# Optimization experiments

Measured on AMD Instinct MI355X. Metric: run time of the kernel, lower is better.

The kernel has to match this reference:

```python
import jax, jax.numpy as jnp
import numpy as np

NHEAD = 16
D_MODEL = 1024
HEAD_DIM = D_MODEL // NHEAD


def setup_inputs() -> dict:
    key = jax.random.key(0)
    k1, k2, k3 = jax.random.split(key, 3)
    x = jax.random.normal(k1, (4, 2048, D_MODEL), dtype=jnp.float32)
    # lecun_normal-like scaling for stability
    w_qkv = jax.random.normal(k2, (D_MODEL, 3 * D_MODEL), dtype=jnp.float32) / np.sqrt(D_MODEL)
    w_out = jax.random.normal(k3, (D_MODEL, D_MODEL), dtype=jnp.float32) / np.sqrt(D_MODEL)
    return {"x": x, "w_qkv": w_qkv, "w_out": w_out}


def reference(x, w_qkv, w_out):
    # Fused QKV projection (self-attention: x_kv = x)
    qkv = x @ w_qkv  # [B, S, 3*D]
    q, k, v = jnp.split(qkv, 3, axis=-1)
    B, S = x.shape[0], x.shape[1]
    # [B, S, H, hd] -> [B, H, S, hd]
    q = jnp.moveaxis(q.reshape(B, S, NHEAD, HEAD_DIM), -2, -3)
    k = jnp.moveaxis(k.reshape(B, S, NHEAD, HEAD_DIM), -2, -3)
    v = jnp.moveaxis(v.reshape(B, S, NHEAD, HEAD_DIM), -2, -3)
    scale = 1.0 / jnp.sqrt(jnp.float32(HEAD_DIM))
    logits = jnp.einsum('bhqd,bhkd->bhqk', q, k) * scale
    weights = jax.nn.softmax(logits, axis=-1)
    out = jnp.einsum('bhqk,bhkd->bhqd', weights, v)  # [B, H, S, hd]
    out = jnp.moveaxis(out, -3, -2).reshape(B, S, D_MODEL)
    return out @ w_out
```

## Files before the change

### kernel.cpp

```cpp
#include <hip/hip_runtime.h>
#include <hip/hip_bf16.h>
#include <math.h>

#define D_MODEL 1024
#define NHEAD   16
#define HEAD_DIM 64
#define BATCH   4
#define SEQ     2048

typedef __attribute__((ext_vector_type(8))) short bf16x8;
typedef __attribute__((ext_vector_type(4))) float f32x4;
typedef __attribute__((ext_vector_type(16))) float f32x16;

__device__ inline ushort f2bf(float f) {
  __hip_bfloat16 h = __float2bfloat16(f);
  return *reinterpret_cast<ushort*>(&h);
}
__device__ inline uint pk2(float a, float b) {
  return (uint)f2bf(a) | ((uint)f2bf(b) << 16);
}
__device__ inline float bf2f(ushort u) {
  return __uint_as_float((uint)u << 16);
}
__device__ inline f32x16 zero16() {
  f32x16 z;
#pragma unroll
  for (int i = 0; i < 16; ++i) z[i] = 0.f;
  return z;
}
__device__ inline float fexp2(float x) { return __builtin_amdgcn_exp2f(x); }

__device__ inline void gld_lds16(const ushort* g, ushort* l) {
  __builtin_amdgcn_global_load_lds(
      (const __attribute__((address_space(1))) void*)g,
      (__attribute__((address_space(3))) void*)l, 16, 0, 0);
}

__global__ __launch_bounds__(256) void fill_f32(float* __restrict__ p, int n, float v) {
  int i = blockIdx.x * 256 + threadIdx.x;
  if (i < n) p[i] = v;
}

__global__ __launch_bounds__(256) void cast_bf16(const float* __restrict__ in,
                                                 ushort* __restrict__ out, int n8) {
  int i = blockIdx.x * 256 + threadIdx.x;
  if (i >= n8) return;
  const float4* p = (const float4*)(in + i * 8);
  float4 a = p[0], b = p[1];
  uint4 o;
  o.x = pk2(a.x, a.y); o.y = pk2(a.z, a.w);
  o.z = pk2(b.x, b.y); o.w = pk2(b.z, b.w);
  ((uint4*)out)[i] = o;
}

__global__ __launch_bounds__(256) void transpose_f32_bf16(const float* __restrict__ in,
                                                          ushort* __restrict__ out,
                                                          int R, int C) {
  __shared__ float tile[32][33];
  int tx = threadIdx.x, ty = threadIdx.y;
  int c0 = blockIdx.x * 32, r0 = blockIdx.y * 32;
#pragma unroll
  for (int k = 0; k < 4; ++k)
    tile[ty + 8 * k][tx] = in[(size_t)(r0 + ty + 8 * k) * C + c0 + tx];
  __syncthreads();
#pragma unroll
  for (int k = 0; k < 4; ++k)
    out[(size_t)(c0 + ty + 8 * k) * R + r0 + tx] = f2bf(tile[tx][ty + 8 * k]);
}

template <typename OutT>
__global__ __launch_bounds__(256) void gemm_mfma(const ushort* __restrict__ A,
                                                 const ushort* __restrict__ BT,
                                                 OutT* __restrict__ C,
                                                 int M, int N, int K) {
  __shared__ ushort As[128 * 32];
  __shared__ ushort Bs[128 * 32];

  const int tid = threadIdx.x;
  const int w = tid >> 6, lane = tid & 63;
  const int quad = lane >> 4, l16 = lane & 15;

  int bx = blockIdx.x, by = blockIdx.y;
  {
    int nwg = gridDim.x * gridDim.y;
    if ((nwg & 7) == 0) {
      int bid = by * gridDim.x + bx;
      int chunk = nwg >> 3;
      bid = (bid & 7) * chunk + (bid >> 3);
      bx = bid % gridDim.x;
      by = bid / gridDim.x;
    }
  }
  const int m0 = by * 128, n0 = bx * 128;
  const int wm = (w & 1) * 64, wn = (w >> 1) * 64;

  f32x4 acc[4][4];
#pragma unroll
  for (int mt = 0; mt < 4; ++mt)
#pragma unroll
    for (int nt = 0; nt < 4; ++nt) acc[mt][nt] = (f32x4){0.f, 0.f, 0.f, 0.f};

  const int c0 = w * 64 + lane;
  const int r0a = c0 >> 2, k0a = (c0 & 3) * 8;
  const int c1 = 256 + c0;
  const int r1a = c1 >> 2, k1a = (c1 & 3) * 8;
  const ushort* a_src0 = A + (size_t)(m0 + r0a) * K + k0a;
  const ushort* a_src1 = A + (size_t)(m0 + r1a) * K + k1a;
  const ushort* b_src0 = BT + (size_t)(n0 + r0a) * K + k0a;
  const ushort* b_src1 = BT + (size_t)(n0 + r1a) * K + k1a;
  ushort* a_dst0 = As + (size_t)w * 512;
  ushort* a_dst1 = As + 2048 + (size_t)w * 512;
  ushort* b_dst0 = Bs + (size_t)w * 512;
  ushort* b_dst1 = Bs + 2048 + (size_t)w * 512;

  for (int k0 = 0; k0 < K; k0 += 32) {
    gld_lds16(a_src0 + k0, a_dst0);
    gld_lds16(a_src1 + k0, a_dst1);
    gld_lds16(b_src0 + k0, b_dst0);
    gld_lds16(b_src1 + k0, b_dst1);
    __syncthreads();

    bf16x8 af[4], bf[4];
#pragma unroll
    for (int mt = 0; mt < 4; ++mt)
      af[mt] = *(const bf16x8*)(As + (wm + mt * 16 + l16) * 32 + quad * 8);
#pragma unroll
    for (int nt = 0; nt < 4; ++nt)
      bf[nt] = *(const bf16x8*)(Bs + (wn + nt * 16 + l16) * 32 + quad * 8);
#pragma unroll
    for (int mt = 0; mt < 4; ++mt)
#pragma unroll
      for (int nt = 0; nt < 4; ++nt)
        acc[mt][nt] = __builtin_amdgcn_mfma_f32_16x16x32_bf16(af[mt], bf[nt], acc[mt][nt], 0, 0, 0);
    __syncthreads();
  }

#pragma unroll
  for (int mt = 0; mt < 4; ++mt) {
#pragma unroll
    for (int nt = 0; nt < 4; ++nt) {
#pragma unroll
      for (int r = 0; r < 4; ++r) {
        size_t idx = (size_t)(m0 + wm + mt * 16 + quad * 4 + r) * N + n0 + wn + nt * 16 + l16;
        if constexpr (sizeof(OutT) == 4) C[idx] = acc[mt][nt][r];
        else                             C[idx] = f2bf(acc[mt][nt][r]);
      }
    }
  }
}

#define KST 72
#define VST 72
#define NT  (SEQ / 64)
__global__ __launch_bounds__(256, 4) void attn_mfma(const ushort* __restrict__ qkv,
                                                    ushort* __restrict__ attn_o) {
  __shared__ ushort Ks[2][64 * KST];
  __shared__ ushort VTs[2][64 * VST];

  const int tid = threadIdx.x;
  const int w = tid >> 6, lane = tid & 63;
  const int q32 = lane & 31, hi = lane >> 5;

  const int f = blockIdx.x;
  const int xcd = f & 7;
  const int j = f >> 3;
  const int qb = j & 15;
  const int hb = ((j >> 4) << 3) | xcd;
  const int h = hb & 15, b = hb >> 4;
  const int q0 = qb * 128;

  const float qscale = 0.125f * 1.44269504088896f;
  bf16x8 qfrag[4];
  {
    const ushort* qrow = qkv + (size_t)(b * SEQ + q0 + w * 32 + q32) * 3072 + h * 64;
#pragma unroll
    for (int dd = 0; dd < 4; ++dd) {
      bf16x8 fq = *(const bf16x8*)(qrow + dd * 16 + hi * 8);
#pragma unroll
      for (int jj = 0; jj < 8; ++jj)
        fq[jj] = (short)f2bf(bf2f((ushort)fq[jj]) * qscale);
      qfrag[dd] = fq;
    }
  }

  f32x16 oacc0 = zero16(), oacc1 = zero16(), lacc = zero16();

  bf16x8 ones;
#pragma unroll
  for (int jj = 0; jj < 8; ++jj) ones[jj] = (short)0x3F80;

  const int sr = tid >> 2, sc = tid & 3;
  const int kp = tid & 31, dg = tid >> 5;

  const size_t kstep = (size_t)64 * 3072;
  const ushort* kbase = qkv + (size_t)(b * SEQ + sr) * 3072 + 1024 + h * 64 + sc * 16;
  const ushort* vbase = qkv + (size_t)(b * SEQ + 2 * kp) * 3072 + 2048 + h * 64 + dg * 8;

  uint4 kreg0, kreg1, vreg0, vreg1;
  {
    const uint4* ks = (const uint4*)kbase;
    kreg0 = ks[0]; kreg1 = ks[1];
    vreg0 = *(const uint4*)vbase;
    vreg1 = *(const uint4*)(vbase + 3072);
    uint4* kdst = (uint4*)(Ks[0] + sr * KST + sc * 16);
    kdst[0] = kreg0; kdst[1] = kreg1;
    const ushort* ae = (const ushort*)&vreg0;
    const ushort* ce = (const ushort*)&vreg1;
#pragma unroll
    for (int jj = 0; jj < 8; ++jj) {
      VTs[0][(dg * 8 + jj) * VST + 2 * kp]     = ae[jj];
      VTs[0][(dg * 8 + jj) * VST + 2 * kp + 1] = ce[jj];
    }
  }

  for (int kt = 0; kt < NT; ++kt) {
    const int cur = kt & 1;
    __syncthreads();

    if (kt + 1 < NT) {
      const uint4* ks = (const uint4*)(kbase + (size_t)(kt + 1) * kstep);
      kreg0 = ks[0]; kreg1 = ks[1];
      vreg0 = *(const uint4*)(vbase + (size_t)(kt + 1) * kstep);
      vreg1 = *(const uint4*)(vbase + (size_t)(kt + 1) * kstep + 3072);
    }

    f32x16 sacc0 = zero16(), sacc1 = zero16();
    __builtin_amdgcn_s_setprio(1);
#pragma unroll
    for (int dd = 0; dd < 4; ++dd) {
      bf16x8 kf0 = *(const bf16x8*)(Ks[cur] + (q32)*KST + dd * 16 + hi * 8);
      bf16x8 kf1 = *(const bf16x8*)(Ks[cur] + (32 + q32) * KST + dd * 16 + hi * 8);
      sacc0 = __builtin_amdgcn_mfma_f32_32x32x16_bf16(kf0, qfrag[dd], sacc0, 0, 0, 0);
      sacc1 = __builtin_amdgcn_mfma_f32_32x32x16_bf16(kf1, qfrag[dd], sacc1, 0, 0, 0);
    }
    __builtin_amdgcn_s_setprio(0);

    bf16x8 pa[4];
#pragma unroll
    for (int kblk = 0; kblk < 2; ++kblk) {
      const f32x16& sacc = kblk ? sacc1 : sacc0;
      uint d0[4], d1[4];
#pragma unroll
      for (int p = 0; p < 4; ++p) {
        d0[p] = pk2(fexp2(sacc[4 * p + 0]), fexp2(sacc[4 * p + 1]));
        d1[p] = pk2(fexp2(sacc[4 * p + 2]), fexp2(sacc[4 * p + 3]));
      }
#pragma unroll
      for (int k2 = 0; k2 < 2; ++k2) {
        uint A0 = d0[2 * k2], B0 = d0[2 * k2 + 1];
        uint A1 = d1[2 * k2], B1 = d1[2 * k2 + 1];
        asm("v_permlane32_swap_b32 %0, %1" : "+v"(A0), "+v"(B0));
        asm("v_permlane32_swap_b32 %0, %1" : "+v"(A1), "+v"(B1));
        uint4 fr = {A0, A1, B0, B1};
        pa[kblk * 2 + k2] = *(bf16x8*)&fr;
        lacc = __builtin_amdgcn_mfma_f32_32x32x16_bf16(pa[kblk * 2 + k2], ones, lacc, 0, 0, 0);
      }
    }

    __builtin_amdgcn_s_setprio(1);
#pragma unroll
    for (int kb2 = 0; kb2 < 4; ++kb2) {
      bf16x8 vf0 = *(const bf16x8*)(VTs[cur] + (q32)*VST + kb2 * 16 + hi * 8);
      bf16x8 vf1 = *(const bf16x8*)(VTs[cur] + (32 + q32) * VST + kb2 * 16 + hi * 8);
      oacc0 = __builtin_amdgcn_mfma_f32_32x32x16_bf16(pa[kb2], vf0, oacc0, 0, 0, 0);
      oacc1 = __builtin_amdgcn_mfma_f32_32x32x16_bf16(pa[kb2], vf1, oacc1, 0, 0, 0);
    }
    __builtin_amdgcn_s_setprio(0);

    if (kt + 1 < NT) {
      uint4* kdst = (uint4*)(Ks[cur ^ 1] + sr * KST + sc * 16);
      kdst[0] = kreg0; kdst[1] = kreg1;
      const ushort* ae = (const ushort*)&vreg0;
      const ushort* ce = (const ushort*)&vreg1;
#pragma unroll
      for (int jj = 0; jj < 8; ++jj) {
        VTs[cur ^ 1][(dg * 8 + jj) * VST + 2 * kp]     = ae[jj];
        VTs[cur ^ 1][(dg * 8 + jj) * VST + 2 * kp + 1] = ce[jj];
      }
    }
  }

#pragma unroll
  for (int p = 0; p < 4; ++p) {
#pragma unroll
    for (int r = 0; r < 4; ++r) {
      int qrow = r + 8 * p + 4 * hi;
      float linv = 1.0f / lacc[4 * p + r];
      ushort* orow = attn_o + (size_t)(b * SEQ + q0 + w * 32 + qrow) * 1024 + h * 64 + q32;
      orow[0]  = f2bf(oacc0[4 * p + r] * linv);
      orow[32] = f2bf(oacc1[4 * p + r] * linv);
    }
  }
}

extern "C" void kernel_launch(void* const* d_in, const int* in_sizes, int n_in,
                              void* d_out, int out_size, void* d_ws, size_t ws_size,
                              hipStream_t stream) {
  bool ok_n  = (n_in == 3);
  bool ok_s0 = ok_n && (in_sizes[0] == 4 * 2048 * 1024);
  bool ok_s1 = ok_n && (in_sizes[1] == 1024 * 3072);
  bool ok_s2 = ok_n && (in_sizes[2] == 1024 * 1024);
  bool ok_o  = (out_size == 4 * 2048 * 1024);
  bool ok_w  = (ws_size >= (size_t)8192 * 3072 * 4);
  if (!(ok_n && ok_s0 && ok_s1 && ok_s2 && ok_o && ok_w)) {
    float c = 64.0f + 1.0f * ok_n + 2.0f * ok_s0 + 4.0f * ok_s1 +
              8.0f * ok_s2 + 16.0f * ok_o + 32.0f * ok_w;
    fill_f32<<<(out_size + 255) / 256, 256, 0, stream>>>((float*)d_out, out_size, c);
    return;
  }

  const float* x     = (const float*)d_in[0];
  const float* w_qkv = (const float*)d_in[1];
  const float* w_out = (const float*)d_in[2];

  char* ws = (char*)d_ws;
  ushort* qkv    = (ushort*)ws;
  ushort* xb     = (ushort*)(ws + (size_t)48 * 1024 * 1024);
  ushort* attn_o = (ushort*)(ws + (size_t)64 * 1024 * 1024);
  ushort* wqkvT  = (ushort*)(ws + (size_t)80 * 1024 * 1024);
  ushort* woutT  = (ushort*)(ws + (size_t)86 * 1024 * 1024);

  cast_bf16<<<dim3(8192 * 1024 / 8 / 256), dim3(256), 0, stream>>>(x, xb, 8192 * 1024 / 8);
  transpose_f32_bf16<<<dim3(3072 / 32, 1024 / 32), dim3(32, 8), 0, stream>>>(w_qkv, wqkvT, 1024, 3072);
  transpose_f32_bf16<<<dim3(1024 / 32, 1024 / 32), dim3(32, 8), 0, stream>>>(w_out, woutT, 1024, 1024);

  gemm_mfma<ushort><<<dim3(3072 / 128, 8192 / 128), dim3(256), 0, stream>>>(
      xb, wqkvT, qkv, 8192, 3072, 1024);

  attn_mfma<<<dim3(1024), dim3(256), 0, stream>>>(qkv, attn_o);

  gemm_mfma<float><<<dim3(1024 / 128, 8192 / 128), dim3(256), 0, stream>>>(
      attn_o, woutT, (float*)d_out, 8192, 1024, 1024);
}
```

Measured before the change: 289.3 us.

## Rewrite GEMM as 256x128 double-buffered tile with swizzled LDS and 8 waves

Replaces the 128x128, 4-wave, single-buffered GEMM with a 256x128 tile computed by 512 threads, a K-step of 64, and two LDS buffers. Global-to-LDS loads for the next K tile are issued before the current tile's MFMAs run, and LDS addresses are XOR-swizzled to avoid bank conflicts. Compute is split into two half-tiles with barriers and s_setprio around the MFMA bursts. This hides global load latency and halves the number of barriers per K, at the cost of more LDS per block (96KB) and fewer workgroups for the smaller output projection.

Result: slower. 304.1 us (+5.1%).

```diff
diff --git a/kernel.cpp b/kernel.cpp
--- a/kernel.cpp
+++ b/kernel.cpp
@@ -68,17 +68,23 @@
     out[(size_t)(c0 + ty + 8 * k) * R + r0 + tx] = f2bf(tile[tx][ty + 8 * k]);
 }
 
+__device__ inline bf16x8 lds_read_swz(const ushort* base, int byteoff) {
+  byteoff ^= ((byteoff >> 9) & 1) << 5;
+  return *(const bf16x8*)((const char*)base + byteoff);
+}
+
 template <typename OutT>
-__global__ __launch_bounds__(256) void gemm_mfma(const ushort* __restrict__ A,
-                                                 const ushort* __restrict__ BT,
-                                                 OutT* __restrict__ C,
-                                                 int M, int N, int K) {
-  __shared__ ushort As[128 * 32];
-  __shared__ ushort Bs[128 * 32];
+__global__ __launch_bounds__(512, 2) void gemm_mfma256(const ushort* __restrict__ A,
+                                                       const ushort* __restrict__ BT,
+                                                       OutT* __restrict__ C,
+                                                       int M, int N, int K) {
+  __shared__ ushort AS[2][256 * 64];
+  __shared__ ushort BS[2][128 * 64];
 
   const int tid = threadIdx.x;
   const int w = tid >> 6, lane = tid & 63;
   const int quad = lane >> 4, l16 = lane & 15;
+  const int wm = w >> 2, wn = w & 3;
 
   int bx = blockIdx.x, by = blockIdx.y;
   {
@@ -91,57 +97,102 @@
       by = bid / gridDim.x;
     }
   }
-  const int m0 = by * 128, n0 = bx * 128;
-  const int wm = (w & 1) * 64, wn = (w >> 1) * 64;
-
-  f32x4 acc[4][4];
-#pragma unroll
-  for (int mt = 0; mt < 4; ++mt)
-#pragma unroll
-    for (int nt = 0; nt < 4; ++nt) acc[mt][nt] = (f32x4){0.f, 0.f, 0.f, 0.f};
-
-  const int c0 = w * 64 + lane;
-  const int r0a = c0 >> 2, k0a = (c0 & 3) * 8;
-  const int c1 = 256 + c0;
-  const int r1a = c1 >> 2, k1a = (c1 & 3) * 8;
-  const ushort* a_src0 = A + (size_t)(m0 + r0a) * K + k0a;
-  const ushort* a_src1 = A + (size_t)(m0 + r1a) * K + k1a;
-  const ushort* b_src0 = BT + (size_t)(n0 + r0a) * K + k0a;
-  const ushort* b_src1 = BT + (size_t)(n0 + r1a) * K + k1a;
-  ushort* a_dst0 = As + (size_t)w * 512;
-  ushort* a_dst1 = As + 2048 + (size_t)w * 512;
-  ushort* b_dst0 = Bs + (size_t)w * 512;
-  ushort* b_dst1 = Bs + 2048 + (size_t)w * 512;
-
-  for (int k0 = 0; k0 < K; k0 += 32) {
-    gld_lds16(a_src0 + k0, a_dst0);
-    gld_lds16(a_src1 + k0, a_dst1);
-    gld_lds16(b_src0 + k0, b_dst0);
-    gld_lds16(b_src1 + k0, b_dst1);
-    __syncthreads();
-
-    bf16x8 af[4], bf[4];
-#pragma unroll
-    for (int mt = 0; mt < 4; ++mt)
-      af[mt] = *(const bf16x8*)(As + (wm + mt * 16 + l16) * 32 + quad * 8);
-#pragma unroll
-    for (int nt = 0; nt < 4; ++nt)
-      bf[nt] = *(const bf16x8*)(Bs + (wn + nt * 16 + l16) * 32 + quad * 8);
-#pragma unroll
-    for (int mt = 0; mt < 4; ++mt)
-#pragma unroll
-      for (int nt = 0; nt < 4; ++nt)
-        acc[mt][nt] = __builtin_amdgcn_mfma_f32_16x16x32_bf16(af[mt], bf[nt], acc[mt][nt], 0, 0, 0);
-    __syncthreads();
-  }
-
-#pragma unroll
-  for (int mt = 0; mt < 4; ++mt) {
-#pragma unroll
-    for (int nt = 0; nt < 4; ++nt) {
+  const int m0 = by * 256, n0 = bx * 128;
+
+  f32x4 acc[8][2];
+#pragma unroll
+  for (int mt = 0; mt < 8; ++mt)
+#pragma unroll
+    for (int nt = 0; nt < 2; ++nt) acc[mt][nt] = (f32x4){0.f, 0.f, 0.f, 0.f};
+
+  const ushort* asrc[4];
+  const ushort* bsrc[2];
+  uint adst[4], bdst[2];
+#pragma unroll
+  for (int i = 0; i < 4; ++i) {
+    int x = (i * 512 + tid) * 16;
+    int sx = x ^ (((x >> 9) & 1) << 5);
+    asrc[i] = A + (size_t)(m0 + (sx >> 7)) * K + ((sx & 127) >> 1);
+    adst[i] = (uint)(i * 512 + w * 64) * 8;
+  }
+#pragma unroll
+  for (int i = 0; i < 2; ++i) {
+    int x = (i * 512 + tid) * 16;
+    int sx = x ^ (((x >> 9) & 1) << 5);
+    bsrc[i] = BT + (size_t)(n0 + (sx >> 7)) * K + ((sx & 127) >> 1);
+    bdst[i] = (uint)(i * 512 + w * 64) * 8;
+  }
+
+  const int NKT = K >> 6;
+
+#pragma unroll
+  for (int i = 0; i < 4; ++i) gld_lds16(asrc[i], AS[0] + adst[i]);
+#pragma unroll
+  for (int i = 0; i < 2; ++i) gld_lds16(bsrc[i], BS[0] + bdst[i]);
+  asm volatile("s_waitcnt vmcnt(0)" ::: "memory");
+  __builtin_amdgcn_s_barrier();
+
+  for (int kt = 0; kt < NKT; ++kt) {
+    const int cur = kt & 1;
+    const int k0n = (kt + 1) << 6;
+
+    if (kt + 1 < NKT) {
+#pragma unroll
+      for (int i = 0; i < 4; ++i) gld_lds16(asrc[i] + k0n, AS[cur ^ 1] + adst[i]);
+#pragma unroll
+      for (int i = 0; i < 2; ++i) gld_lds16(bsrc[i] + k0n, BS[cur ^ 1] + bdst[i]);
+    }
+
+    bf16x8 af[4][2], bf[2][2];
+#pragma unroll
+    for (int f = 0; f < 4; ++f)
+#pragma unroll
+      for (int kk = 0; kk < 2; ++kk)
+        af[f][kk] = lds_read_swz(AS[cur], (wm * 128 + f * 16 + l16) * 128 + kk * 64 + quad * 16);
+#pragma unroll
+    for (int fn = 0; fn < 2; ++fn)
+#pragma unroll
+      for (int kk = 0; kk < 2; ++kk)
+        bf[fn][kk] = lds_read_swz(BS[cur], (wn * 32 + fn * 16 + l16) * 128 + kk * 64 + quad * 16);
+    __builtin_amdgcn_s_barrier();
+    __builtin_amdgcn_s_setprio(1);
+#pragma unroll
+    for (int f = 0; f < 4; ++f)
+#pragma unroll
+      for (int fn = 0; fn < 2; ++fn)
+#pragma unroll
+        for (int kk = 0; kk < 2; ++kk)
+          acc[f][fn] = __builtin_amdgcn_mfma_f32_16x16x32_bf16(af[f][kk], bf[fn][kk], acc[f][fn], 0, 0, 0);
+    __builtin_amdgcn_s_setprio(0);
+    __builtin_amdgcn_s_barrier();
+
+#pragma unroll
+    for (int f = 0; f < 4; ++f)
+#pragma unroll
+      for (int kk = 0; kk < 2; ++kk)
+        af[f][kk] = lds_read_swz(AS[cur], (wm * 128 + 64 + f * 16 + l16) * 128 + kk * 64 + quad * 16);
+    __builtin_amdgcn_s_barrier();
+    __builtin_amdgcn_s_setprio(1);
+#pragma unroll
+    for (int f = 0; f < 4; ++f)
+#pragma unroll
+      for (int fn = 0; fn < 2; ++fn)
+#pragma unroll
+        for (int kk = 0; kk < 2; ++kk)
+          acc[4 + f][fn] = __builtin_amdgcn_mfma_f32_16x16x32_bf16(af[f][kk], bf[fn][kk], acc[4 + f][fn], 0, 0, 0);
+    __builtin_amdgcn_s_setprio(0);
+
+    asm volatile("s_waitcnt vmcnt(0)" ::: "memory");
+    __builtin_amdgcn_s_barrier();
+  }
+
+#pragma unroll
+  for (int mt = 0; mt < 8; ++mt) {
+#pragma unroll
+    for (int nt = 0; nt < 2; ++nt) {
 #pragma unroll
       for (int r = 0; r < 4; ++r) {
-        size_t idx = (size_t)(m0 + wm + mt * 16 + quad * 4 + r) * N + n0 + wn + nt * 16 + l16;
+        size_t idx = (size_t)(m0 + wm * 128 + mt * 16 + quad * 4 + r) * N + n0 + wn * 32 + nt * 16 + l16;
         if constexpr (sizeof(OutT) == 4) C[idx] = acc[mt][nt][r];
         else                             C[idx] = f2bf(acc[mt][nt][r]);
       }
@@ -324,11 +375,11 @@
   transpose_f32_bf16<<<dim3(3072 / 32, 1024 / 32), dim3(32, 8), 0, stream>>>(w_qkv, wqkvT, 1024, 3072);
   transpose_f32_bf16<<<dim3(1024 / 32, 1024 / 32), dim3(32, 8), 0, stream>>>(w_out, woutT, 1024, 1024);
 
-  gemm_mfma<ushort><<<dim3(3072 / 128, 8192 / 128), dim3(256), 0, stream>>>(
+  gemm_mfma256<ushort><<<dim3(3072 / 128, 8192 / 256), dim3(512), 0, stream>>>(
       xb, wqkvT, qkv, 8192, 3072, 1024);
 
   attn_mfma<<<dim3(1024), dim3(256), 0, stream>>>(qkv, attn_o);
 
-  gemm_mfma<float><<<dim3(1024 / 128, 8192 / 128), dim3(256), 0, stream>>>(
+  gemm_mfma256<float><<<dim3(1024 / 128, 8192 / 256), dim3(512), 0, stream>>>(
       attn_o, woutT, (float*)d_out, 8192, 1024, 1024);
 }
```
